# Kernel tuning notes

Hardware: AMD Instinct MI355X
Metric: run time of the kernel (lower is better)

The kernel has to match this reference:

```python
import jax, jax.numpy as jnp
import numpy as np

B, S = 8, 1024          # sequences, uniform seqlen (cu_seqlens = arange(B+1)*S)
H, HID = 16, 2048       # num_heads, hidden_size
D = HID // H            # head_size = 128


def setup_inputs() -> dict:
    key = jax.random.key(0)
    k0, k1, k2 = jax.random.split(key, 3)
    T = B * S
    hidden_states = jax.random.normal(k0, (T, HID), jnp.float32)
    # FastLinear after prepare_weights stores weight transposed: [in, out]
    w_attn = jax.random.normal(k1, (HID, HID + 2 * D), jnp.float32) * 0.02
    b_attn = jnp.zeros((HID + 2 * D,), jnp.float32)
    w_proj = jax.random.normal(k2, (HID, HID), jnp.float32) * 0.02
    b_proj = jnp.zeros((HID,), jnp.float32)
    cu_seqlens = jnp.arange(B + 1, dtype=jnp.int32) * S
    layer_past = jnp.zeros((T, 2, 1, D), jnp.float32)
    return {
        "hidden_states": hidden_states,
        "w_attn": w_attn,
        "b_attn": b_attn,
        "w_proj": w_proj,
        "b_proj": b_proj,
        "cu_seqlens": cu_seqlens,
        "max_s": S,
        "layer_past": layer_past,
    }


def reference(hidden_states, w_attn, b_attn, w_proj, b_proj, cu_seqlens, max_s, layer_past):
    # Prefill branch: causal MQA flash attention; layer_past is written (cache)
    # but the returned output does not depend on it.
    scale = D ** -0.5
    qkv = hidden_states @ w_attn + b_attn                 # [T, HID + 2D]
    q = qkv[:, :HID].reshape(B, S, H, D)                  # [B,S,H,D]
    kv = qkv[:, HID:].reshape(B, S, 2, D)
    k = kv[:, :, 0]                                       # [B,S,D] single KV head
    v = kv[:, :, 1]                                       # [B,S,D]
    scores = jnp.einsum('bqhd,bkd->bhqk', q, k) * scale   # [B,H,S,S]
    causal = jnp.tril(jnp.ones((S, S), dtype=bool))
    scores = jnp.where(causal, scores, jnp.finfo(scores.dtype).min)
    probs = jax.nn.softmax(scores, axis=-1)
    attn = jnp.einsum('bhqk,bkd->bqhd', probs, v)         # [B,S,H,D]
    attn = attn.reshape(B * S, HID)
    return attn @ w_proj + b_proj                         # [T, HID]
```

## Files before the change

kernel.cpp:

```cpp
#include <hip/hip_runtime.h>
#include <hip/hip_bf16.h>

typedef __hip_bfloat16 bf16;
typedef __attribute__((ext_vector_type(8))) __bf16 bf16x8;
typedef __attribute__((ext_vector_type(4))) float f32x4;
typedef __attribute__((ext_vector_type(16))) float f32x16;
typedef __attribute__((ext_vector_type(8))) short s16x8;
typedef __attribute__((ext_vector_type(4))) unsigned u32x4;

#define B_    8
#define S_    1024
#define H_    16
#define D_    128
#define HID_  2048
#define NQKV_ 2304
#define T_    8192

__device__ __forceinline__ void gload_lds16(const void* g, void* l) {
  __builtin_amdgcn_global_load_lds((const __attribute__((address_space(1))) void*)g,
                                   (__attribute__((address_space(3))) void*)l, 16, 0, 0);
}

__device__ __forceinline__ unsigned pack_bf16(float lo, float hi) {
  return ((unsigned)__bfloat16_as_ushort(__float2bfloat16(hi)) << 16) |
         (unsigned)__bfloat16_as_ushort(__float2bfloat16(lo));
}

__global__ void cast_bf16_kernel(const float* __restrict__ src, bf16* __restrict__ dst, int n8) {
  const int i = blockIdx.x * 256 + threadIdx.x;
  if (i >= n8) return;
  const float4 a = ((const float4*)src)[2 * i];
  const float4 b = ((const float4*)src)[2 * i + 1];
  s16x8 o;
  o[0] = (short)__bfloat16_as_ushort(__float2bfloat16(a.x));
  o[1] = (short)__bfloat16_as_ushort(__float2bfloat16(a.y));
  o[2] = (short)__bfloat16_as_ushort(__float2bfloat16(a.z));
  o[3] = (short)__bfloat16_as_ushort(__float2bfloat16(a.w));
  o[4] = (short)__bfloat16_as_ushort(__float2bfloat16(b.x));
  o[5] = (short)__bfloat16_as_ushort(__float2bfloat16(b.y));
  o[6] = (short)__bfloat16_as_ushort(__float2bfloat16(b.z));
  o[7] = (short)__bfloat16_as_ushort(__float2bfloat16(b.w));
  ((s16x8*)dst)[i] = o;
}

__global__ void transpose_cast_kernel(const float* __restrict__ src, bf16* __restrict__ dst,
                                      int R, int C) {
  __shared__ float tile[32][33];
  const int tx = threadIdx.x & 31, ty = threadIdx.x >> 5;
  const int rt = blockIdx.y * 32, ct = blockIdx.x * 32;
#pragma unroll
  for (int k = 0; k < 4; ++k)
    tile[ty + 8 * k][tx] = src[(size_t)(rt + ty + 8 * k) * C + ct + tx];
  __syncthreads();
#pragma unroll
  for (int k = 0; k < 4; ++k)
    dst[(size_t)(ct + ty + 8 * k) * R + rt + tx] = __float2bfloat16(tile[tx][ty + 8 * k]);
}

__global__ void transpose_v_kernel(const bf16* __restrict__ QKV, bf16* __restrict__ Vt) {
  __shared__ short t[64][72];
  const int kt = blockIdx.x, dt = blockIdx.y, b = blockIdx.z;
  const int r = threadIdx.x >> 3;
  const int c8 = (threadIdx.x & 7) * 8;
#pragma unroll
  for (int p = 0; p < 2; ++p) {
    const int row = p * 32 + r;
    const s16x8 v = *(const s16x8*)(QKV + (size_t)(b * S_ + kt * 64 + row) * NQKV_ +
                                    HID_ + D_ + dt * 64 + c8);
    *(s16x8*)&t[row][c8] = v;
  }
  __syncthreads();
#pragma unroll
  for (int p = 0; p < 2; ++p) {
    const int drow = p * 32 + r;
    s16x8 o;
#pragma unroll
    for (int j = 0; j < 8; ++j) o[j] = t[c8 + j][drow];
    *(s16x8*)(Vt + (size_t)(b * D_ + dt * 64 + drow) * S_ + kt * 64 + c8) = o;
  }
}

template <bool OUT_F32>
__global__ __launch_bounds__(256, 2) void gemm_kernel(const bf16* __restrict__ A,
                                                      const bf16* __restrict__ Bt,
                                                      const float* __restrict__ bias,
                                                      void* __restrict__ Cout,
                                                      int M, int N, int K) {
  __shared__ char lds[65536];
  const int tid = threadIdx.x;
  const int lane = tid & 63;
  const int wave = tid >> 6;

  const int gx = gridDim.x;
  const int lid = blockIdx.y * gx + blockIdx.x;
  const int cpx = (gx * gridDim.y) >> 3;
  const int swz = (lid & 7) * cpx + (lid >> 3);
  const int bn = swz % gx, bm = swz / gx;

  const int lrow = lane & 15, lk = lane >> 4;
  const int rbase = (wave >> 1) * 64;
  const int nbase = (wave & 1) * 64;
  f32x4 acc[4][4] = {};

  int srow[4], scol[4];
#pragma unroll
  for (int o = 0; o < 4; ++o) {
    const int X = o * 4096 + tid * 16;
    const int r = X >> 7, Y = X & 127;
    srow[o] = r;
    scol[o] = Y ^ ((r & 7) << 4);
  }

  const char* Ab = (const char*)A + (size_t)(bm * 128) * K * 2;
  const char* Bb = (const char*)Bt + (size_t)(bn * 128) * K * 2;

#define G_STAGE(buf, kt_)                                                              \
  _Pragma("unroll") for (int o = 0; o < 4; ++o)                                        \
      gload_lds16(Ab + (size_t)srow[o] * (K * 2) + (size_t)(kt_) * 128 + scol[o],      \
                  lds + (buf) + o * 4096 + tid * 16);                                  \
  _Pragma("unroll") for (int o = 0; o < 4; ++o)                                        \
      gload_lds16(Bb + (size_t)srow[o] * (K * 2) + (size_t)(kt_) * 128 + scol[o],      \
                  lds + (buf) + 16384 + o * 4096 + tid * 16);

  G_STAGE(0, 0);

  const int nkt = K >> 6;
  for (int kt = 0; kt < nkt; ++kt) {
    const int cur = (kt & 1) * 32768;
    if (kt < nkt - 1) {
      G_STAGE(cur ^ 32768, kt + 1);
      asm volatile("s_waitcnt vmcnt(8)" ::: "memory");
    } else {
      asm volatile("s_waitcnt vmcnt(0)" ::: "memory");
    }
    __builtin_amdgcn_s_barrier();

    bf16x8 af[4][2], bfr[4][2];
#pragma unroll
    for (int mi = 0; mi < 4; ++mi) {
      const int row = rbase + mi * 16 + lrow;
#pragma unroll
      for (int kk = 0; kk < 2; ++kk)
        af[mi][kk] =
            *(const bf16x8*)(lds + cur + row * 128 + ((kk * 64 + lk * 16) ^ ((row & 7) << 4)));
    }
#pragma unroll
    for (int ni = 0; ni < 4; ++ni) {
      const int row = nbase + ni * 16 + lrow;
#pragma unroll
      for (int kk = 0; kk < 2; ++kk)
        bfr[ni][kk] = *(const bf16x8*)(lds + cur + 16384 + row * 128 +
                                       ((kk * 64 + lk * 16) ^ ((row & 7) << 4)));
    }
#pragma unroll
    for (int kk = 0; kk < 2; ++kk)
#pragma unroll
      for (int mi = 0; mi < 4; ++mi)
#pragma unroll
        for (int ni = 0; ni < 4; ++ni)
          acc[mi][ni] =
              __builtin_amdgcn_mfma_f32_16x16x32_bf16(af[mi][kk], bfr[ni][kk], acc[mi][ni], 0, 0, 0);
    __builtin_amdgcn_s_barrier();
  }
#undef G_STAGE

#pragma unroll
  for (int ni = 0; ni < 4; ++ni) {
    const int col = bn * 128 + nbase + ni * 16 + lrow;
    const float bv = bias[col];
#pragma unroll
    for (int mi = 0; mi < 4; ++mi) {
      const int row0 = bm * 128 + rbase + mi * 16 + lk * 4;
#pragma unroll
      for (int r = 0; r < 4; ++r) {
        const float v = acc[mi][ni][r] + bv;
        if (OUT_F32)
          ((float*)Cout)[(size_t)(row0 + r) * N + col] = v;
        else
          ((bf16*)Cout)[(size_t)(row0 + r) * N + col] = __float2bfloat16(v);
      }
    }
  }
}

__global__ __launch_bounds__(256, 2) void attn_kernel(const bf16* __restrict__ QKV,
                                                      const bf16* __restrict__ Vt,
                                                      bf16* __restrict__ aout) {
  const int qt = gridDim.x - 1 - blockIdx.x;
  const int h = blockIdx.y;
  const int b = blockIdx.z;
  const int tid = threadIdx.x;
  const int l = tid & 63;
  const int w = tid >> 6;
  const int ql = l & 31;
  const int hi = l >> 5;

  __shared__ char lds[49152];

  const char* qkv_b = (const char*)QKV + (size_t)b * S_ * (NQKV_ * 2);
  const char* vt_b = (const char*)Vt + (size_t)b * D_ * S_ * 2;

  int kr[4], kc[4], vr[4], vc[4];
#pragma unroll
  for (int o = 0; o < 4; ++o) {
    const int X = w * 4096 + o * 1024 + l * 16;
    const int r = X >> 8;
    kr[o] = r;
    kc[o] = (X & 255) ^ ((r & 15) << 4);
    const int d = X >> 7;
    vr[o] = d;
    vc[o] = (X & 127) ^ ((d & 7) << 4);
  }

#define STAGE_K(kb_off, kt_)                                                          \
  _Pragma("unroll") for (int o = 0; o < 4; ++o)                                       \
      gload_lds16(qkv_b + (size_t)((kt_) * 64 + kr[o]) * (NQKV_ * 2) + HID_ * 2 +     \
                      kc[o],                                                          \
                  lds + (kb_off) + w * 4096 + o * 1024);
#define STAGE_V(kt_)                                                                  \
  _Pragma("unroll") for (int o = 0; o < 4; ++o)                                       \
      gload_lds16(vt_b + (size_t)vr[o] * (S_ * 2) + (kt_) * 128 + vc[o],              \
                  lds + 32768 + w * 4096 + o * 1024);

#pragma unroll
  for (int o = 0; o < 8; ++o) {
    const int X = w * 8192 + o * 1024 + l * 16;
    const int r = X >> 8;
    const int cb = (X & 255) ^ ((r & 15) << 4);
    gload_lds16(qkv_b + (size_t)(qt * 128 + r) * (NQKV_ * 2) + h * 256 + cb, lds + X);
  }
  asm volatile("s_waitcnt vmcnt(0)" ::: "memory");
  __builtin_amdgcn_s_barrier();

  bf16x8 qf[8];
  {
    const int qrow = w * 32 + ql;
#pragma unroll
    for (int ds = 0; ds < 8; ++ds)
      qf[ds] = *(const bf16x8*)(lds + qrow * 256 + ((ds * 32 + hi * 16) ^ ((qrow & 15) << 4)));
  }
  asm volatile("s_waitcnt lgkmcnt(0)" ::: "memory");
  __builtin_amdgcn_sched_barrier(0);
  __builtin_amdgcn_s_barrier();

  STAGE_K(0, 0);

  const float scale = 0.08838834764831845f;
  const int qglob = qt * 128 + w * 32 + ql;
  float mrun = -1e30f, lrun = 0.f;
  f32x16 Oacc[4] = {};

  const int nkt = 2 * qt + 2;
  for (int kt = 0; kt < nkt; ++kt) {
    const int kb = (kt & 1) * 16384;
    STAGE_V(kt);
    if (kt < nkt - 1) {
      STAGE_K(kb ^ 16384, kt + 1);
      asm volatile("s_waitcnt vmcnt(8)" ::: "memory");
    } else {
      asm volatile("s_waitcnt vmcnt(4)" ::: "memory");
    }
    __builtin_amdgcn_s_barrier();
    __builtin_amdgcn_sched_barrier(0);

    const bool skip = (64 * kt >= 128 * qt + 32 * w + 32);
    bf16x8 pa[4];
    if (!skip) {
      const bool need_mask = (64 * kt + 63 > 128 * qt + 32 * w);

      f32x16 s0 = {}, s1 = {};
      __builtin_amdgcn_s_setprio(1);
#pragma unroll
      for (int ds = 0; ds < 8; ++ds) {
        const int krow = ql;
        const bf16x8 kf =
            *(const bf16x8*)(lds + kb + krow * 256 + ((ds * 32 + hi * 16) ^ ((krow & 15) << 4)));
        s0 = __builtin_amdgcn_mfma_f32_32x32x16_bf16(kf, qf[ds], s0, 0, 0, 0);
      }
#pragma unroll
      for (int ds = 0; ds < 8; ++ds) {
        const int krow = 32 + ql;
        const bf16x8 kf =
            *(const bf16x8*)(lds + kb + krow * 256 + ((ds * 32 + hi * 16) ^ ((krow & 15) << 4)));
        s1 = __builtin_amdgcn_mfma_f32_32x32x16_bf16(kf, qf[ds], s1, 0, 0, 0);
      }
      __builtin_amdgcn_s_setprio(0);

#pragma unroll
      for (int r = 0; r < 16; ++r) {
        const int krl = (r & 3) + 8 * (r >> 2) + 4 * hi;
        float v0 = s0[r] * scale, v1 = s1[r] * scale;
        if (need_mask) {
          if (64 * kt + krl > qglob) v0 = -1e30f;
          if (64 * kt + 32 + krl > qglob) v1 = -1e30f;
        }
        s0[r] = v0;
        s1[r] = v1;
      }

      float a0 = -1e30f, a1 = -1e30f, a2 = -1e30f, a3 = -1e30f;
#pragma unroll
      for (int r = 0; r < 16; r += 4) {
        a0 = fmaxf(a0, fmaxf(s0[r], s1[r]));
        a1 = fmaxf(a1, fmaxf(s0[r + 1], s1[r + 1]));
        a2 = fmaxf(a2, fmaxf(s0[r + 2], s1[r + 2]));
        a3 = fmaxf(a3, fmaxf(s0[r + 3], s1[r + 3]));
      }
      float tmax = fmaxf(fmaxf(a0, a1), fmaxf(a2, a3));
      tmax = fmaxf(tmax, __shfl_xor(tmax, 32));

      if (!__all(tmax <= mrun + 8.f)) {
        const float mn = fmaxf(mrun, tmax);
        const float corr = __expf(mrun - mn);
        mrun = mn;
        lrun *= corr;
#pragma unroll
        for (int r = 0; r < 16; ++r) {
          const float cq = __shfl(corr, (r & 3) + 8 * (r >> 2) + 4 * hi);
#pragma unroll
          for (int dt = 0; dt < 4; ++dt) Oacc[dt][r] *= cq;
        }
      }

      float b0 = 0.f, b1 = 0.f, b2 = 0.f, b3 = 0.f;
#pragma unroll
      for (int r = 0; r < 16; r += 4) {
        s0[r] = __expf(s0[r] - mrun);
        s1[r] = __expf(s1[r] - mrun);
        b0 += s0[r] + s1[r];
        s0[r + 1] = __expf(s0[r + 1] - mrun);
        s1[r + 1] = __expf(s1[r + 1] - mrun);
        b1 += s0[r + 1] + s1[r + 1];
        s0[r + 2] = __expf(s0[r + 2] - mrun);
        s1[r + 2] = __expf(s1[r + 2] - mrun);
        b2 += s0[r + 2] + s1[r + 2];
        s0[r + 3] = __expf(s0[r + 3] - mrun);
        s1[r + 3] = __expf(s1[r + 3] - mrun);
        b3 += s0[r + 3] + s1[r + 3];
      }
      float rs = (b0 + b1) + (b2 + b3);
      rs += __shfl_xor(rs, 32);
      lrun += rs;

      unsigned c[16], xc[16];
#pragma unroll
      for (int m = 0; m < 8; ++m) {
        c[m] = pack_bf16(s0[2 * m], s0[2 * m + 1]);
        c[8 + m] = pack_bf16(s1[2 * m], s1[2 * m + 1]);
      }
#pragma unroll
      for (int m = 0; m < 16; ++m) xc[m] = (unsigned)__shfl_xor((int)c[m], 32);

#pragma unroll
      for (int kh = 0; kh < 2; ++kh) {
        const int base = 8 * kh;
        u32x4 f0, f1;
        f0[0] = hi ? xc[base + 2] : c[base + 0];
        f0[1] = hi ? xc[base + 3] : c[base + 1];
        f0[2] = hi ? c[base + 2] : xc[base + 0];
        f0[3] = hi ? c[base + 3] : xc[base + 1];
        f1[0] = hi ? xc[base + 6] : c[base + 4];
        f1[1] = hi ? xc[base + 7] : c[base + 5];
        f1[2] = hi ? c[base + 6] : xc[base + 4];
        f1[3] = hi ? c[base + 7] : xc[base + 5];
        pa[2 * kh] = __builtin_bit_cast(bf16x8, f0);
        pa[2 * kh + 1] = __builtin_bit_cast(bf16x8, f1);
      }
    }

    if (kt < nkt - 1)
      asm volatile("s_waitcnt vmcnt(4)" ::: "memory");
    else
      asm volatile("s_waitcnt vmcnt(0)" ::: "memory");
    __builtin_amdgcn_s_barrier();
    __builtin_amdgcn_sched_barrier(0);

    if (!skip) {
      __builtin_amdgcn_s_setprio(1);
#pragma unroll
      for (int dt = 0; dt < 4; ++dt) {
        const int vrow = dt * 32 + ql;
#pragma unroll
        for (int ks = 0; ks < 4; ++ks) {
          const bf16x8 vf = *(const bf16x8*)(lds + 32768 + vrow * 128 +
                                             ((ks * 32 + hi * 16) ^ ((vrow & 7) << 4)));
          Oacc[dt] = __builtin_amdgcn_mfma_f32_32x32x16_bf16(pa[ks], vf, Oacc[dt], 0, 0, 0);
        }
      }
      __builtin_amdgcn_s_setprio(0);
    }
    __builtin_amdgcn_s_barrier();
  }

#pragma unroll
  for (int r = 0; r < 16; ++r) {
    const int qi = (r & 3) + 8 * (r >> 2) + 4 * hi;
    const float lr = __shfl(lrun, qi);
    const float inv = 1.0f / lr;
    const int token = b * S_ + qt * 128 + w * 32 + qi;
    bf16* orow = aout + (size_t)token * HID_ + h * D_;
#pragma unroll
    for (int dt = 0; dt < 4; ++dt)
      orow[dt * 32 + ql] = __float2bfloat16(Oacc[dt][r] * inv);
  }
#undef STAGE_K
#undef STAGE_V
}

extern "C" void kernel_launch(void* const* d_in, const int* in_sizes, int n_in,
                              void* d_out, int out_size, void* d_ws, size_t ws_size,
                              hipStream_t stream) {
  const float* hidden = (const float*)d_in[0];
  const float* w_attn = (const float*)d_in[1];
  const float* b_attn = (const float*)d_in[2];
  const float* w_proj = (const float*)d_in[3];
  const float* b_proj = (const float*)d_in[4];

  char* ws = (char*)d_ws;
  char* dob = (char*)d_out;

  bf16* Xbf = (bf16*)ws;
  bf16* WpT = (bf16*)(ws + 33554432);
  bf16* QKV = (bf16*)dob;
  bf16* WaT = (bf16*)(dob + 37748736);
  bf16* Vt = (bf16*)(dob + 50331648);

  cast_bf16_kernel<<<(T_ * HID_) / 8 / 256, 256, 0, stream>>>(hidden, Xbf, (T_ * HID_) / 8);
  transpose_cast_kernel<<<dim3(NQKV_ / 32, HID_ / 32), 256, 0, stream>>>(w_attn, WaT, HID_, NQKV_);
  transpose_cast_kernel<<<dim3(HID_ / 32, HID_ / 32), 256, 0, stream>>>(w_proj, WpT, HID_, HID_);

  gemm_kernel<false><<<dim3(NQKV_ / 128, T_ / 128), 256, 0, stream>>>(
      Xbf, WaT, b_attn, QKV, T_, NQKV_, HID_);

  transpose_v_kernel<<<dim3(S_ / 64, D_ / 64, B_), 256, 0, stream>>>(QKV, Vt);

  attn_kernel<<<dim3(S_ / 128, H_, B_), 256, 0, stream>>>(QKV, Vt, Xbf);

  gemm_kernel<true><<<dim3(HID_ / 128, T_ / 128), 256, 0, stream>>>(
      Xbf, WpT, b_proj, (float*)d_out, T_, HID_, HID_);
}
```

Baseline: 296.2 us.

## Enlarge GEMM tiles to 256x256 with 8-wave phased MFMA schedule

Both projection GEMMs move from 128x128 tiles with 4 waves to 256x256 tiles with 8 waves, using 128KB of LDS and a two-deep prefetch of the K slices. Each K step is split into four MFMA phases with staggered LDS fragment reads, barriers and s_setprio raising wave priority around the MFMA bursts. The intent is more data reuse per loaded tile and better overlap of LDS reads with matrix math. The trade-off is a large LDS footprint, which limits occupancy to one block per CU. The QKV GEMM now launches 288 blocks, which leaves a partial second wave on the GPU.

```diff
diff --git a/kernel.cpp b/kernel.cpp
--- a/kernel.cpp
+++ b/kernel.cpp
@@ -81,15 +81,18 @@
 }
 
 template <bool OUT_F32>
-__global__ __launch_bounds__(256, 2) void gemm_kernel(const bf16* __restrict__ A,
+__global__ __launch_bounds__(512, 2) void gemm_kernel(const bf16* __restrict__ A,
                                                       const bf16* __restrict__ Bt,
                                                       const float* __restrict__ bias,
                                                       void* __restrict__ Cout,
                                                       int M, int N, int K) {
-  __shared__ char lds[65536];
+  __shared__ char lds[131072];
   const int tid = threadIdx.x;
   const int lane = tid & 63;
   const int wave = tid >> 6;
+  const int wm = wave >> 2;
+  const int wn = wave & 3;
+  const int lrow = lane & 15, lk = lane >> 4;
 
   const int gx = gridDim.x;
   const int lid = blockIdx.y * gx + blockIdx.x;
@@ -97,83 +100,105 @@
   const int swz = (lid & 7) * cpx + (lid >> 3);
   const int bn = swz % gx, bm = swz / gx;
 
-  const int lrow = lane & 15, lk = lane >> 4;
-  const int rbase = (wave >> 1) * 64;
-  const int nbase = (wave & 1) * 64;
-  f32x4 acc[4][4] = {};
+  f32x4 acc[8][4] = {};
 
   int srow[4], scol[4];
 #pragma unroll
   for (int o = 0; o < 4; ++o) {
-    const int X = o * 4096 + tid * 16;
+    const int X = o * 8192 + tid * 16;
     const int r = X >> 7, Y = X & 127;
     srow[o] = r;
     scol[o] = Y ^ ((r & 7) << 4);
   }
 
-  const char* Ab = (const char*)A + (size_t)(bm * 128) * K * 2;
-  const char* Bb = (const char*)Bt + (size_t)(bn * 128) * K * 2;
-
-#define G_STAGE(buf, kt_)                                                              \
-  _Pragma("unroll") for (int o = 0; o < 4; ++o)                                        \
-      gload_lds16(Ab + (size_t)srow[o] * (K * 2) + (size_t)(kt_) * 128 + scol[o],      \
-                  lds + (buf) + o * 4096 + tid * 16);                                  \
-  _Pragma("unroll") for (int o = 0; o < 4; ++o)                                        \
-      gload_lds16(Bb + (size_t)srow[o] * (K * 2) + (size_t)(kt_) * 128 + scol[o],      \
-                  lds + (buf) + 16384 + o * 4096 + tid * 16);
-
-  G_STAGE(0, 0);
-
+  const char* Ab = (const char*)A + (size_t)(bm * 256) * K * 2;
+  const char* Bb = (const char*)Bt + (size_t)(bn * 256) * K * 2;
+
+#define STG(cbuf, kt_)                                                                  \
+  _Pragma("unroll") for (int o = 0; o < 4; ++o)                                         \
+      gload_lds16(Ab + (size_t)srow[o] * (K * 2) + (size_t)(kt_) * 128 + scol[o],       \
+                  lds + (cbuf) + o * 8192 + tid * 16);                                  \
+  _Pragma("unroll") for (int o = 0; o < 4; ++o)                                         \
+      gload_lds16(Bb + (size_t)srow[o] * (K * 2) + (size_t)(kt_) * 128 + scol[o],       \
+                  lds + (cbuf) + 32768 + o * 8192 + tid * 16);
+
+#define RD_A(cbuf, msub)                                                                \
+  _Pragma("unroll") for (int mi = 0; mi < 4; ++mi)                                      \
+  _Pragma("unroll") for (int ks = 0; ks < 2; ++ks) {                                    \
+    const int row = wm * 128 + (msub) * 64 + mi * 16 + lrow;                            \
+    afr[mi][ks] = *(const bf16x8*)(lds + (cbuf) + row * 128 +                           \
+                                   ((ks * 64 + lk * 16) ^ ((row & 7) << 4)));           \
+  }
+#define RD_B(cbuf, nlo)                                                                 \
+  _Pragma("unroll") for (int ni = 0; ni < 2; ++ni)                                      \
+  _Pragma("unroll") for (int ks = 0; ks < 2; ++ks) {                                    \
+    const int row = wn * 64 + ((nlo) + ni) * 16 + lrow;                                 \
+    bfrg[(nlo) + ni][ks] = *(const bf16x8*)(lds + (cbuf) + 32768 + row * 128 +          \
+                                            ((ks * 64 + lk * 16) ^ ((row & 7) << 4)));  \
+  }
+#define LGKM0()                                           \
+  asm volatile("s_waitcnt lgkmcnt(0)" ::: "memory");      \
+  __builtin_amdgcn_sched_barrier(0);
+#define PH_MFMA(MLO, NLO)                                                               \
+  __builtin_amdgcn_s_setprio(1);                                                        \
+  _Pragma("unroll") for (int ks = 0; ks < 2; ++ks)                                      \
+  _Pragma("unroll") for (int mi = 0; mi < 4; ++mi)                                      \
+  _Pragma("unroll") for (int ni = 0; ni < 2; ++ni)                                      \
+    acc[(MLO) + mi][(NLO) + ni] = __builtin_amdgcn_mfma_f32_16x16x32_bf16(              \
+        afr[mi][ks], bfrg[(NLO) + ni][ks], acc[(MLO) + mi][(NLO) + ni], 0, 0, 0);       \
+  __builtin_amdgcn_s_setprio(0);
+
+  STG(0, 0);
+  STG(65536, 1);
+  asm volatile("s_waitcnt vmcnt(8)" ::: "memory");
+  __builtin_amdgcn_s_barrier();
+
+  bf16x8 afr[4][2], bfrg[4][2];
   const int nkt = K >> 6;
   for (int kt = 0; kt < nkt; ++kt) {
-    const int cur = (kt & 1) * 32768;
-    if (kt < nkt - 1) {
-      G_STAGE(cur ^ 32768, kt + 1);
+    const int cb = (kt & 1) * 65536;
+    RD_A(cb, 0);
+    RD_B(cb, 0);
+    __builtin_amdgcn_s_barrier();
+    LGKM0();
+    PH_MFMA(0, 0);
+    __builtin_amdgcn_s_barrier();
+    RD_B(cb, 2);
+    __builtin_amdgcn_s_barrier();
+    LGKM0();
+    PH_MFMA(0, 2);
+    __builtin_amdgcn_s_barrier();
+    RD_A(cb, 1);
+    __builtin_amdgcn_s_barrier();
+    LGKM0();
+    PH_MFMA(4, 0);
+    __builtin_amdgcn_s_barrier();
+    if (kt + 2 < nkt) {
+      STG(cb, kt + 2);
       asm volatile("s_waitcnt vmcnt(8)" ::: "memory");
-    } else {
+    } else if (kt == nkt - 2) {
       asm volatile("s_waitcnt vmcnt(0)" ::: "memory");
     }
     __builtin_amdgcn_s_barrier();
-
-    bf16x8 af[4][2], bfr[4][2];
-#pragma unroll
-    for (int mi = 0; mi < 4; ++mi) {
-      const int row = rbase + mi * 16 + lrow;
-#pragma unroll
-      for (int kk = 0; kk < 2; ++kk)
-        af[mi][kk] =
-            *(const bf16x8*)(lds + cur + row * 128 + ((kk * 64 + lk * 16) ^ ((row & 7) << 4)));
-    }
-#pragma unroll
-    for (int ni = 0; ni < 4; ++ni) {
-      const int row = nbase + ni * 16 + lrow;
-#pragma unroll
-      for (int kk = 0; kk < 2; ++kk)
-        bfr[ni][kk] = *(const bf16x8*)(lds + cur + 16384 + row * 128 +
-                                       ((kk * 64 + lk * 16) ^ ((row & 7) << 4)));
-    }
-#pragma unroll
-    for (int kk = 0; kk < 2; ++kk)
-#pragma unroll
-      for (int mi = 0; mi < 4; ++mi)
-#pragma unroll
-        for (int ni = 0; ni < 4; ++ni)
-          acc[mi][ni] =
-              __builtin_amdgcn_mfma_f32_16x16x32_bf16(af[mi][kk], bfr[ni][kk], acc[mi][ni], 0, 0, 0);
-    __builtin_amdgcn_s_barrier();
-  }
-#undef G_STAGE
-
-#pragma unroll
-  for (int ni = 0; ni < 4; ++ni) {
-    const int col = bn * 128 + nbase + ni * 16 + lrow;
+    PH_MFMA(4, 2);
+    __builtin_amdgcn_s_barrier();
+  }
+#undef STG
+#undef RD_A
+#undef RD_B
+#undef LGKM0
+#undef PH_MFMA
+
+#pragma unroll
+  for (int an = 0; an < 4; ++an) {
+    const int col = bn * 256 + wn * 64 + an * 16 + lrow;
     const float bv = bias[col];
 #pragma unroll
-    for (int mi = 0; mi < 4; ++mi) {
-      const int row0 = bm * 128 + rbase + mi * 16 + lk * 4;
+    for (int am = 0; am < 8; ++am) {
+      const int row0 = bm * 256 + wm * 128 + am * 16 + lk * 4;
 #pragma unroll
       for (int r = 0; r < 4; ++r) {
-        const float v = acc[mi][ni][r] + bv;
+        const float v = acc[am][an][r] + bv;
         if (OUT_F32)
           ((float*)Cout)[(size_t)(row0 + r) * N + col] = v;
         else
@@ -429,13 +454,13 @@
   transpose_cast_kernel<<<dim3(NQKV_ / 32, HID_ / 32), 256, 0, stream>>>(w_attn, WaT, HID_, NQKV_);
   transpose_cast_kernel<<<dim3(HID_ / 32, HID_ / 32), 256, 0, stream>>>(w_proj, WpT, HID_, HID_);
 
-  gemm_kernel<false><<<dim3(NQKV_ / 128, T_ / 128), 256, 0, stream>>>(
+  gemm_kernel<false><<<dim3(NQKV_ / 256, T_ / 256), 512, 0, stream>>>(
       Xbf, WaT, b_attn, QKV, T_, NQKV_, HID_);
 
   transpose_v_kernel<<<dim3(S_ / 64, D_ / 64, B_), 256, 0, stream>>>(QKV, Vt);
 
   attn_kernel<<<dim3(S_ / 128, H_, B_), 256, 0, stream>>>(QKV, Vt, Xbf);
 
-  gemm_kernel<true><<<dim3(HID_ / 128, T_ / 128), 256, 0, stream>>>(
+  gemm_kernel<true><<<dim3(HID_ / 256, T_ / 256), 512, 0, stream>>>(
       Xbf, WpT, b_proj, (float*)d_out, T_, HID_, HID_);
 }
```

Result: slower. 331.2 us (+11.8%).
